# Performance work log

Hardware: AMD Instinct MI355X
Metric: run time of the kernel (lower is better)

Reference implementation:

```python
import jax, jax.numpy as jnp
import numpy as np

LN_EPS = 1e-5


def setup_inputs() -> dict:
    key = jax.random.key(0)
    ks = jax.random.split(key, 5)
    N, E, D = 50000, 600000, 128
    x = jax.random.normal(ks[0], (N, D), dtype=jnp.float32)
    edge_index = jax.random.randint(ks[1], (2, E), 0, N, dtype=jnp.int64)
    W_l = jax.random.normal(ks[2], (D, D), dtype=jnp.float32) * (1.0 / np.sqrt(D))
    b_l = jnp.zeros((D,), dtype=jnp.float32)
    W_r = jax.random.normal(ks[3], (D, D), dtype=jnp.float32) * (1.0 / np.sqrt(D))
    gamma = jnp.ones((D,), dtype=jnp.float32)
    beta = jnp.zeros((D,), dtype=jnp.float32)
    return {"x": x, "edge_index": edge_index, "W_l": W_l, "b_l": b_l,
            "W_r": W_r, "gamma": gamma, "beta": beta}


def reference(x, edge_index, W_l, b_l, W_r, gamma, beta):
    # SAGEConv (mean aggregation): out = lin_l(mean_{j in N(i)} x_j) + lin_r(x_i)
    N = x.shape[0]
    src, dst = edge_index[0], edge_index[1]
    msg = x[src]                                                # (E, D) gather
    agg = jax.ops.segment_sum(msg, dst, num_segments=N)         # (N, D) scatter-add
    cnt = jax.ops.segment_sum(jnp.ones_like(dst, dtype=x.dtype), dst, num_segments=N)
    mean = agg / jnp.maximum(cnt, 1.0)[:, None]
    h = mean @ W_l.T + b_l + x @ W_r.T                          # (N, D)
    # LayerNorm over feature dim
    mu = jnp.mean(h, axis=-1, keepdims=True)
    var = jnp.mean(jnp.square(h - mu), axis=-1, keepdims=True)
    h = (h - mu) * jax.lax.rsqrt(var + LN_EPS) * gamma + beta
    # ReLU; Dropout is identity in eval mode
    return jax.nn.relu(h)
```

## Files before the change

kernel.cpp:

```cpp
#include <hip/hip_runtime.h>
#include <stdint.h>

#define DIM 128
#define LN_EPS 1e-5f
#define BROWS 32
#define BINB 256
#define NT1 1024
#define SCAP 8
#define NBKT_MAX 1600
#define LELLS 56
#define LOVF 64
#define OVFCAP 4096
#define ATS 264
#define PINIT ((int)0xAAAAAAAA)

typedef __attribute__((ext_vector_type(8))) short bf16x8;
typedef __attribute__((ext_vector_type(4))) float f32x4;
typedef __attribute__((ext_vector_type(4))) uint32_t u32x4;

static __device__ __forceinline__ uint16_t f2bf(float f) {
    uint32_t u = __float_as_uint(f);
    return (uint16_t)((u + 0x7fffu + ((u >> 16) & 1u)) >> 16);
}
static __device__ __forceinline__ float bf_lo(uint32_t w) {
    return __uint_as_float(w << 16);
}
static __device__ __forceinline__ float bf_hi(uint32_t w) {
    return __uint_as_float(w & 0xffff0000u);
}

#define CONS(Q, PR, A) do { float _p = (PR); \
    A[0] = fmaf(_p, bf_lo(Q[0]), A[0]); A[1] = fmaf(_p, bf_hi(Q[0]), A[1]); \
    A[2] = fmaf(_p, bf_lo(Q[1]), A[2]); A[3] = fmaf(_p, bf_hi(Q[1]), A[3]); \
    A[4] = fmaf(_p, bf_lo(Q[2]), A[4]); A[5] = fmaf(_p, bf_hi(Q[2]), A[5]); \
    A[6] = fmaf(_p, bf_lo(Q[3]), A[6]); A[7] = fmaf(_p, bf_hi(Q[3]), A[7]); } while (0)

__global__ __launch_bounds__(NT1) void bin_kernel(
    const int* __restrict__ ei,
    const float* __restrict__ x,
    const float* __restrict__ Wl,
    const float* __restrict__ Wr,
    uint8_t* __restrict__ cnt, uint32_t* __restrict__ bedge,
    int* __restrict__ novf, int* __restrict__ ovf,
    uint16_t* __restrict__ x16, uint16_t* __restrict__ wc,
    int E, int N, int nbkt)
{
    __shared__ int hist[NBKT_MAX];
    const int t = threadIdx.x, b = blockIdx.x;

    for (int i = t; i < nbkt; i += NT1) hist[i] = 0;
    __syncthreads();

    const int chunk = (E + BINB - 1) / BINB;
    const int e0 = b * chunk;
    const int e1 = (e0 + chunk < E) ? e0 + chunk : E;

    for (int e = e0 + t; e < e1; e += NT1)
        atomicAdd(&hist[ei[E + e] >> 5], 1);
    __syncthreads();

    for (int i = t; i < nbkt; i += NT1) {
        int c = hist[i];
        cnt[(size_t)i * BINB + b] = (uint8_t)(c > 255 ? 255 : c);
        hist[i] = 0;
    }
    __syncthreads();

    for (int e = e0 + t; e < e1; e += NT1) {
        int src = ei[e];
        int dst = ei[E + e];
        int bkt = dst >> 5;
        int r = atomicAdd(&hist[bkt], 1);
        if (r < SCAP) {
            bedge[((size_t)bkt * BINB + b) * SCAP + r] =
                ((uint32_t)(dst & 31) << 27) | (uint32_t)src;
        } else {
            int q = atomicAdd(novf, 1) - PINIT;
            if (q >= 0 && q < OVFCAP) { ovf[2 * q] = dst; ovf[2 * q + 1] = src; }
        }
    }

    {
        int tid = b * NT1 + t, nth = BINB * NT1;
        int nxp = (N * DIM) >> 1;
        for (int i = tid; i < nxp; i += nth) {
            float2 v = *(const float2*)(x + 2 * i);
            uint32_t u = ((uint32_t)f2bf(v.y) << 16) | (uint32_t)f2bf(v.x);
            ((uint32_t*)x16)[i] = u;
        }
        for (int i = tid; i < DIM * 256; i += nth) {
            int d = i >> 8, k = i & 255;
            float v = (k < DIM) ? Wl[d * DIM + k] : Wr[d * DIM + (k - DIM)];
            wc[i] = f2bf(v);
        }
    }
}

__global__ __launch_bounds__(256, 4) void fused_kernel(
    const uint16_t* __restrict__ x16,
    const uint8_t* __restrict__ cnt,
    const uint32_t* __restrict__ bedge,
    const int* __restrict__ novf,
    const int* __restrict__ ovf,
    const uint16_t* __restrict__ wc,
    const float* __restrict__ bl,
    const float* __restrict__ gma,
    const float* __restrict__ bta,
    float* __restrict__ out,
    int N, int E)
{
    __shared__ int ell_s[BROWS][LELLS];
    __shared__ int cnt_s[BROWS];
    __shared__ int lovf_s[LOVF];
    __shared__ int nlovf_s;
    __shared__ __align__(16) uint16_t atile[2][16 * ATS];
    __shared__ float pln[2][16][2][2];

    const int t    = threadIdx.x;
    const int lane = t & 63;
    const int w    = t >> 6;
    const int p    = w >> 1;
    const int h    = w & 1;
    const int tile_row0 = blockIdx.x * BROWS + p * 16;
    const int grow0     = tile_row0 + h * 8;
    const int lb        = p * 16 + h * 8;

    if (t < BROWS) cnt_s[t] = 0;
    if (t == BROWS) nlovf_s = 0;
    __syncthreads();

    {
        int c = cnt[(size_t)blockIdx.x * BINB + t];
        c = (c < SCAP) ? c : SCAP;
        const uint32_t* sp = bedge + ((size_t)blockIdx.x * BINB + t) * SCAP;
        for (int r = 0; r < c; ++r) {
            uint32_t pk = sp[r];
            int local = pk >> 27;
            int rr = atomicAdd(&cnt_s[local], 1);
            if (rr < LELLS) ell_s[local][rr] = (int)(pk & 0x07FFFFFF);
            else {
                int q = atomicAdd(&nlovf_s, 1);
                if (q < LOVF) lovf_s[q] = (int)pk;
            }
        }
    }
    __syncthreads();

    const int rr4 = lane >> 4;
    const int dq  = lane & 15;
    const uint32_t dqo = (uint32_t)dq * 16u;
    const int r0l = lb + rr4;
    const int r1l = lb + 4 + rr4;
    int dg0 = cnt_s[r0l];
    int dg1 = cnt_s[r1l];
    const int nl0 = dg0 < LELLS ? dg0 : LELLS;
    const int nl1 = dg1 < LELLS ? dg1 : LELLS;

    int mx = 0;
    #pragma unroll
    for (int r = 0; r < 8; ++r) {
        int d = __builtin_amdgcn_readfirstlane(cnt_s[lb + r]);
        int tt = d < LELLS ? d : LELLS;
        mx = (tt > mx) ? tt : mx;
    }

    float a0[8], a1[8];
    #pragma unroll
    for (int k = 0; k < 8; ++k) { a0[k] = 0.0f; a1[k] = 0.0f; }

    const uint64_t xb64 = (uint64_t)(uintptr_t)x16;
    const int* rl0 = ell_s[r0l];
    const int* rl1 = ell_s[r1l];

    auto fetch = [&](int jj, int nl, const int* rowlist) -> uint32_t {
        int slot = (jj < nl) ? jj : 0;
        uint32_t v = (uint32_t)rowlist[slot];
        return (jj < nl) ? ((v << 8) | dqo) : dqo;
    };

#define GLD4(dst, vo) \
    asm volatile("global_load_dwordx4 %0, %1, %2 sc0" \
                 : "=&v"(dst) : "v"(vo), "s"(xb64))

    u32x4 qA0, qA1, qB0, qB1;
    if (mx > 0) {
        uint32_t vo0 = fetch(0, nl0, rl0);
        uint32_t vo1 = fetch(0, nl1, rl1);
        GLD4(qA0, vo0); GLD4(qA1, vo1);
        for (int j = 0; j < mx; j += 2) {
            int jb = j + 1;
            vo0 = fetch(jb, nl0, rl0); vo1 = fetch(jb, nl1, rl1);
            GLD4(qB0, vo0); GLD4(qB1, vo1);
            asm volatile("s_waitcnt vmcnt(2)" ::: "memory");
            __builtin_amdgcn_sched_barrier(0);
            CONS(qA0, (j < nl0) ? 1.0f : 0.0f, a0);
            CONS(qA1, (j < nl1) ? 1.0f : 0.0f, a1);
            int jc = j + 2;
            vo0 = fetch(jc, nl0, rl0); vo1 = fetch(jc, nl1, rl1);
            GLD4(qA0, vo0); GLD4(qA1, vo1);
            asm volatile("s_waitcnt vmcnt(2)" ::: "memory");
            __builtin_amdgcn_sched_barrier(0);
            if (jb < mx) {
                CONS(qB0, (jb < nl0) ? 1.0f : 0.0f, a0);
                CONS(qB1, (jb < nl1) ? 1.0f : 0.0f, a1);
            }
        }
        asm volatile("s_waitcnt vmcnt(0)" ::: "memory");
        __builtin_amdgcn_sched_barrier(0);
    }

    {
        int nl = __builtin_amdgcn_readfirstlane(nlovf_s);
        nl = (nl < 0) ? 0 : (nl > LOVF ? LOVF : nl);
        for (int i = 0; i < nl; ++i) {
            uint32_t pk = (uint32_t)lovf_s[i];
            int local = pk >> 27;
            if (local >= lb && local < lb + 8) {
                int srco = (int)(pk & 0x07FFFFFF);
                u32x4 qq = *(const u32x4*)(x16 + (size_t)srco * DIM + 8 * dq);
                CONS(qq, (local == r0l) ? 1.0f : 0.0f, a0);
                CONS(qq, (local == r1l) ? 1.0f : 0.0f, a1);
            }
        }
    }

    {
        int no = __builtin_amdgcn_readfirstlane(novf[0]) - PINIT;
        no = (no < 0) ? 0 : (no > OVFCAP ? OVFCAP : no);
        for (int i = 0; i < no; ++i) {
            int dsto = __builtin_amdgcn_readfirstlane(ovf[2 * i]);
            int srco = __builtin_amdgcn_readfirstlane(ovf[2 * i + 1]);
            if (dsto >= grow0 && dsto < grow0 + 8) {
                u32x4 qq = *(const u32x4*)(x16 + (size_t)srco * DIM + 8 * dq);
                int h0 = (dsto == grow0 + rr4) ? 1 : 0;
                int h1 = (dsto == grow0 + 4 + rr4) ? 1 : 0;
                CONS(qq, h0 ? 1.0f : 0.0f, a0);
                CONS(qq, h1 ? 1.0f : 0.0f, a1);
                dg0 += h0; dg1 += h1;
            }
        }
    }

    {
        uint16_t* at = atile[p];
        float rc0 = (dg0 > 0) ? (1.0f / (float)dg0) : 0.0f;
        float rc1 = (dg1 > 0) ? (1.0f / (float)dg1) : 0.0f;
        int lr0 = h * 8 + rr4;
        int lr1 = h * 8 + 4 + rr4;
        u32x4 w0, w1;
        #pragma unroll
        for (int i = 0; i < 4; ++i) {
            w0[i] = ((uint32_t)f2bf(a0[2 * i + 1] * rc0) << 16) | f2bf(a0[2 * i] * rc0);
            w1[i] = ((uint32_t)f2bf(a1[2 * i + 1] * rc1) << 16) | f2bf(a1[2 * i] * rc1);
        }
        *(u32x4*)&at[lr0 * ATS + 8 * dq] = w0;
        *(u32x4*)&at[lr1 * ATS + 8 * dq] = w1;
        int row0g = grow0 + rr4;     int rs0 = (row0g < N) ? row0g : 0;
        int row1g = grow0 + 4 + rr4; int rs1 = (row1g < N) ? row1g : 0;
        u32x4 xv0 = *(const u32x4*)(x16 + (size_t)rs0 * DIM + 8 * dq);
        u32x4 xv1 = *(const u32x4*)(x16 + (size_t)rs1 * DIM + 8 * dq);
        *(u32x4*)&at[lr0 * ATS + 128 + 8 * dq] = xv0;
        *(u32x4*)&at[lr1 * ATS + 128 + 8 * dq] = xv1;
    }
    __syncthreads();

    const int nsub = lane & 15;
    const int quad = lane >> 4;
    const uint16_t* at = atile[p];

    f32x4 acc[4];
    #pragma unroll
    for (int tt = 0; tt < 4; ++tt) {
        float b = bl[(h * 4 + tt) * 16 + nsub];
        acc[tt] = (f32x4){b, b, b, b};
    }

    #pragma unroll
    for (int c = 0; c < 8; ++c) {
        bf16x8 af = *(const bf16x8*)&at[nsub * ATS + c * 32 + quad * 8];
        #pragma unroll
        for (int tt = 0; tt < 4; ++tt) {
            int tg = h * 4 + tt;
            bf16x8 bfr = *(const bf16x8*)&wc[(size_t)(tg * 16 + nsub) * 256 + c * 32 + quad * 8];
            acc[tt] = __builtin_amdgcn_mfma_f32_16x16x32_bf16(af, bfr, acc[tt], 0, 0, 0);
        }
    }

    #pragma unroll
    for (int i = 0; i < 4; ++i) {
        float s = 0.0f, q = 0.0f;
        #pragma unroll
        for (int tt = 0; tt < 4; ++tt) {
            float v = acc[tt][i];
            s += v;
            q += v * v;
        }
        #pragma unroll
        for (int off = 1; off < 16; off <<= 1) {
            s += __shfl_xor(s, off, 64);
            q += __shfl_xor(q, off, 64);
        }
        if (nsub == 0) {
            pln[p][quad * 4 + i][h][0] = s;
            pln[p][quad * 4 + i][h][1] = q;
        }
    }
    __syncthreads();

    #pragma unroll
    for (int i = 0; i < 4; ++i) {
        int lrow = quad * 4 + i;
        float s = pln[p][lrow][0][0] + pln[p][lrow][1][0];
        float q = pln[p][lrow][0][1] + pln[p][lrow][1][1];
        float mu = s * (1.0f / 128.0f);
        float var = q * (1.0f / 128.0f) - mu * mu;
        float rs = rsqrtf(fmaxf(var, 0.0f) + LN_EPS);
        int grow = tile_row0 + lrow;
        if (grow < N) {
            float* op = out + (size_t)grow * DIM;
            #pragma unroll
            for (int tt = 0; tt < 4; ++tt) {
                int f = (h * 4 + tt) * 16 + nsub;
                float o = fmaxf((acc[tt][i] - mu) * rs * gma[f] + bta[f], 0.0f);
                op[f] = o;
            }
        }
    }
}

extern "C" void kernel_launch(void* const* d_in, const int* in_sizes, int n_in,
                              void* d_out, int out_size, void* d_ws, size_t ws_size,
                              hipStream_t stream) {
    const float* x  = (const float*)d_in[0];
    const int* ei   = (const int*)d_in[1];
    const float* Wl = (const float*)d_in[2];
    const float* bl = (const float*)d_in[3];
    const float* Wr = (const float*)d_in[4];
    const float* ga = (const float*)d_in[5];
    const float* be = (const float*)d_in[6];
    float* out = (float*)d_out;

    int N = in_sizes[0] / DIM;
    int E = in_sizes[1] / 2;
    int nbkt = (N + BROWS - 1) / BROWS;

    uint8_t* cnt    = (uint8_t*)d_ws;
    int* novf       = (int*)(cnt + (size_t)nbkt * BINB);
    uint16_t* wc    = (uint16_t*)(novf + 16);
    uint16_t* x16   = wc + DIM * 256;
    uint32_t* bedge = (uint32_t*)(x16 + (size_t)N * DIM);
    int* ovf        = (int*)(bedge + (size_t)nbkt * BINB * SCAP);

    bin_kernel<<<BINB, NT1, 0, stream>>>(
        ei, x, Wl, Wr, cnt, bedge, novf, ovf, x16, wc, E, N, nbkt);

    fused_kernel<<<nbkt, 256, 0, stream>>>(
        x16, cnt, bedge, novf, ovf, wc, bl, ga, be, out, N, E);
}
```

Before: 156.9 us.

## Gather neighbor features as per-row int8 with scales, deepen gather pipeline

The bin kernel now also quantizes each x row to int8 with a per-row absmax scale. The fused kernel gathers these 8-byte int8 chunks plus a scale instead of 16-byte bf16 chunks, and dequantizes them inside the accumulation FMA. The gather loop becomes three-stage, and the change also lowers SCAP and raises the occupancy hint. This halves the gather traffic, which dominates the cost, at the price of int8 quantization error in the mean aggregation and an extra scale load per edge.

```diff
diff --git a/kernel.cpp b/kernel.cpp
--- a/kernel.cpp
+++ b/kernel.cpp
@@ -6,7 +6,7 @@
 #define BROWS 32
 #define BINB 256
 #define NT1 1024
-#define SCAP 8
+#define SCAP 6
 #define NBKT_MAX 1600
 #define LELLS 56
 #define LOVF 64
@@ -16,7 +16,9 @@
 
 typedef __attribute__((ext_vector_type(8))) short bf16x8;
 typedef __attribute__((ext_vector_type(4))) float f32x4;
+typedef __attribute__((ext_vector_type(2))) float f32x2;
 typedef __attribute__((ext_vector_type(4))) uint32_t u32x4;
+typedef __attribute__((ext_vector_type(2))) uint32_t u32x2;
 
 static __device__ __forceinline__ uint16_t f2bf(float f) {
     uint32_t u = __float_as_uint(f);
@@ -34,6 +36,18 @@
     A[2] = fmaf(_p, bf_lo(Q[1]), A[2]); A[3] = fmaf(_p, bf_hi(Q[1]), A[3]); \
     A[4] = fmaf(_p, bf_lo(Q[2]), A[4]); A[5] = fmaf(_p, bf_hi(Q[2]), A[5]); \
     A[6] = fmaf(_p, bf_lo(Q[3]), A[6]); A[7] = fmaf(_p, bf_hi(Q[3]), A[7]); } while (0)
+
+#define CONS8(Q, PS, A) do { float _s = (PS); uint32_t _w; \
+    _w = Q.x; \
+    A[0] = fmaf(_s, (float)(int8_t)(_w),       A[0]); \
+    A[1] = fmaf(_s, (float)(int8_t)(_w >> 8),  A[1]); \
+    A[2] = fmaf(_s, (float)(int8_t)(_w >> 16), A[2]); \
+    A[3] = fmaf(_s, (float)(int8_t)(_w >> 24), A[3]); \
+    _w = Q.y; \
+    A[4] = fmaf(_s, (float)(int8_t)(_w),       A[4]); \
+    A[5] = fmaf(_s, (float)(int8_t)(_w >> 8),  A[5]); \
+    A[6] = fmaf(_s, (float)(int8_t)(_w >> 16), A[6]); \
+    A[7] = fmaf(_s, (float)(int8_t)(_w >> 24), A[7]); } while (0)
 
 __global__ __launch_bounds__(NT1) void bin_kernel(
     const int* __restrict__ ei,
@@ -42,7 +56,8 @@
     const float* __restrict__ Wr,
     uint8_t* __restrict__ cnt, uint32_t* __restrict__ bedge,
     int* __restrict__ novf, int* __restrict__ ovf,
-    uint16_t* __restrict__ x16, uint16_t* __restrict__ wc,
+    uint16_t* __restrict__ x16, uint8_t* __restrict__ x8,
+    float* __restrict__ scales, uint16_t* __restrict__ wc,
     int E, int N, int nbkt)
 {
     __shared__ int hist[NBKT_MAX];
@@ -81,13 +96,28 @@
     }
 
     {
+        const int lane = t & 63;
+        const int gw = (b * NT1 + t) >> 6;
+        const int nw = (BINB * NT1) >> 6;
+        for (int r = gw; r < N; r += nw) {
+            f32x2 v = *(const f32x2*)(x + (size_t)r * DIM + 2 * lane);
+            uint32_t u = ((uint32_t)f2bf(v.y) << 16) | (uint32_t)f2bf(v.x);
+            ((uint32_t*)x16)[(size_t)r * 64 + lane] = u;
+            float am = fmaxf(fabsf(v.x), fabsf(v.y));
+            #pragma unroll
+            for (int off = 1; off < 64; off <<= 1)
+                am = fmaxf(am, __shfl_xor(am, off, 64));
+            float inv = (am > 0.0f) ? (127.0f / am) : 0.0f;
+            int q0 = (int)rintf(v.x * inv);
+            int q1 = (int)rintf(v.y * inv);
+            *(uint16_t*)(x8 + (size_t)r * DIM + 2 * lane) =
+                (uint16_t)(((uint32_t)(q1 & 0xff) << 8) | (uint32_t)(q0 & 0xff));
+            if (lane == 0) scales[r] = (am > 0.0f) ? (am / 127.0f) : 0.0f;
+        }
+    }
+
+    {
         int tid = b * NT1 + t, nth = BINB * NT1;
-        int nxp = (N * DIM) >> 1;
-        for (int i = tid; i < nxp; i += nth) {
-            float2 v = *(const float2*)(x + 2 * i);
-            uint32_t u = ((uint32_t)f2bf(v.y) << 16) | (uint32_t)f2bf(v.x);
-            ((uint32_t*)x16)[i] = u;
-        }
         for (int i = tid; i < DIM * 256; i += nth) {
             int d = i >> 8, k = i & 255;
             float v = (k < DIM) ? Wl[d * DIM + k] : Wr[d * DIM + (k - DIM)];
@@ -96,8 +126,10 @@
     }
 }
 
-__global__ __launch_bounds__(256, 4) void fused_kernel(
+__global__ __launch_bounds__(256, 6) void fused_kernel(
     const uint16_t* __restrict__ x16,
+    const uint8_t* __restrict__ x8,
+    const float* __restrict__ scales,
     const uint8_t* __restrict__ cnt,
     const uint32_t* __restrict__ bedge,
     const int* __restrict__ novf,
@@ -148,7 +180,6 @@
 
     const int rr4 = lane >> 4;
     const int dq  = lane & 15;
-    const uint32_t dqo = (uint32_t)dq * 16u;
     const int r0l = lb + rr4;
     const int r1l = lb + 4 + rr4;
     int dg0 = cnt_s[r0l];
@@ -168,42 +199,55 @@
     #pragma unroll
     for (int k = 0; k < 8; ++k) { a0[k] = 0.0f; a1[k] = 0.0f; }
 
-    const uint64_t xb64 = (uint64_t)(uintptr_t)x16;
+    const uint64_t xq64 = (uint64_t)(uintptr_t)x8;
+    const uint64_t sc64 = (uint64_t)(uintptr_t)scales;
     const int* rl0 = ell_s[r0l];
     const int* rl1 = ell_s[r1l];
-
-    auto fetch = [&](int jj, int nl, const int* rowlist) -> uint32_t {
+    const uint32_t dqo8 = (uint32_t)dq * 8u;
+
+    auto fet8 = [&](int jj, int nl, const int* rowlist) -> uint32_t {
         int slot = (jj < nl) ? jj : 0;
         uint32_t v = (uint32_t)rowlist[slot];
-        return (jj < nl) ? ((v << 8) | dqo) : dqo;
+        return (jj < nl) ? ((v << 7) | dqo8) : dqo8;
     };
-
-#define GLD4(dst, vo) \
-    asm volatile("global_load_dwordx4 %0, %1, %2 sc0" \
-                 : "=&v"(dst) : "v"(vo), "s"(xb64))
-
-    u32x4 qA0, qA1, qB0, qB1;
+    auto fets = [&](int jj, int nl, const int* rowlist) -> uint32_t {
+        int slot = (jj < nl) ? jj : 0;
+        return ((uint32_t)rowlist[slot]) << 2;
+    };
+
+#define GLD2(dst, vo) \
+    asm volatile("global_load_dwordx2 %0, %1, %2 sc0" \
+                 : "=&v"(dst) : "v"(vo), "s"(xq64))
+#define GLDS(dst, vo) \
+    asm volatile("global_load_dword %0, %1, %2" \
+                 : "=&v"(dst) : "v"(vo), "s"(sc64))
+#define ISSUE(QG0, QG1, S0, S1, jj) do { \
+    uint32_t _v0 = fet8(jj, nl0, rl0), _v1 = fet8(jj, nl1, rl1); \
+    uint32_t _s0 = fets(jj, nl0, rl0), _s1 = fets(jj, nl1, rl1); \
+    GLD2(QG0, _v0); GLD2(QG1, _v1); GLDS(S0, _s0); GLDS(S1, _s1); } while (0)
+#define CONSUME(QG0, QG1, S0, S1, jj) do { \
+    float _p0 = (jj < nl0) ? S0 : 0.0f; \
+    float _p1 = (jj < nl1) ? S1 : 0.0f; \
+    CONS8(QG0, _p0, a0); CONS8(QG1, _p1, a1); } while (0)
+
+    u32x2 qA0, qA1, qB0, qB1, qC0, qC1;
+    float sA0, sA1, sB0, sB1, sC0, sC1;
     if (mx > 0) {
-        uint32_t vo0 = fetch(0, nl0, rl0);
-        uint32_t vo1 = fetch(0, nl1, rl1);
-        GLD4(qA0, vo0); GLD4(qA1, vo1);
-        for (int j = 0; j < mx; j += 2) {
-            int jb = j + 1;
-            vo0 = fetch(jb, nl0, rl0); vo1 = fetch(jb, nl1, rl1);
-            GLD4(qB0, vo0); GLD4(qB1, vo1);
-            asm volatile("s_waitcnt vmcnt(2)" ::: "memory");
+        ISSUE(qA0, qA1, sA0, sA1, 0);
+        ISSUE(qB0, qB1, sB0, sB1, 1);
+        for (int j = 0; j < mx; j += 3) {
+            ISSUE(qC0, qC1, sC0, sC1, j + 2);
+            asm volatile("s_waitcnt vmcnt(8)" ::: "memory");
             __builtin_amdgcn_sched_barrier(0);
-            CONS(qA0, (j < nl0) ? 1.0f : 0.0f, a0);
-            CONS(qA1, (j < nl1) ? 1.0f : 0.0f, a1);
-            int jc = j + 2;
-            vo0 = fetch(jc, nl0, rl0); vo1 = fetch(jc, nl1, rl1);
-            GLD4(qA0, vo0); GLD4(qA1, vo1);
-            asm volatile("s_waitcnt vmcnt(2)" ::: "memory");
+            CONSUME(qA0, qA1, sA0, sA1, j);
+            ISSUE(qA0, qA1, sA0, sA1, j + 3);
+            asm volatile("s_waitcnt vmcnt(8)" ::: "memory");
             __builtin_amdgcn_sched_barrier(0);
-            if (jb < mx) {
-                CONS(qB0, (jb < nl0) ? 1.0f : 0.0f, a0);
-                CONS(qB1, (jb < nl1) ? 1.0f : 0.0f, a1);
-            }
+            if (j + 1 < mx) CONSUME(qB0, qB1, sB0, sB1, j + 1);
+            ISSUE(qB0, qB1, sB0, sB1, j + 4);
+            asm volatile("s_waitcnt vmcnt(8)" ::: "memory");
+            __builtin_amdgcn_sched_barrier(0);
+            if (j + 2 < mx) CONSUME(qC0, qC1, sC0, sC1, j + 2);
         }
         asm volatile("s_waitcnt vmcnt(0)" ::: "memory");
         __builtin_amdgcn_sched_barrier(0);
@@ -348,12 +392,14 @@
     int* novf       = (int*)(cnt + (size_t)nbkt * BINB);
     uint16_t* wc    = (uint16_t*)(novf + 16);
     uint16_t* x16   = wc + DIM * 256;
-    uint32_t* bedge = (uint32_t*)(x16 + (size_t)N * DIM);
+    float* scales   = (float*)(x16 + (size_t)N * DIM);
+    uint8_t* x8     = (uint8_t*)(scales + N);
+    uint32_t* bedge = (uint32_t*)(x8 + (size_t)N * DIM);
     int* ovf        = (int*)(bedge + (size_t)nbkt * BINB * SCAP);
 
     bin_kernel<<<BINB, NT1, 0, stream>>>(
-        ei, x, Wl, Wr, cnt, bedge, novf, ovf, x16, wc, E, N, nbkt);
+        ei, x, Wl, Wr, cnt, bedge, novf, ovf, x16, x8, scales, wc, E, N, nbkt);
 
     fused_kernel<<<nbkt, 256, 0, stream>>>(
-        x16, cnt, bedge, novf, ovf, wc, bl, ga, be, out, N, E);
-}
+        x16, x8, scales, cnt, bedge, novf, ovf, wc, bl, ga, be, out, N, E);
+}
```

New measurement: 212.8 us. 1.36x slower.
